# Kernel tuning notes

Hardware: AMD Instinct MI355X
Metric: run time of the kernel (lower is better)

## Reference

```python
import jax, jax.numpy as jnp
import numpy as np

N_NODES = 100000
N_EDGES = 1600000
N_FEAT = 48
N_EDGE_FEAT = 16
HIDDEN = 128


def setup_inputs() -> dict:
    key = jax.random.key(0)
    ks = jax.random.split(key, 8)
    tot = 2 * N_FEAT + N_EDGE_FEAT  # 112
    s1 = 1.0 / np.sqrt(tot)
    s2 = 1.0 / np.sqrt(HIDDEN)
    return {
        "x": jax.random.normal(ks[0], (N_NODES, N_FEAT), dtype=jnp.float32),
        "edge_index": jax.random.randint(ks[1], (2, N_EDGES), 0, N_NODES, dtype=jnp.int64),
        "edge_feat": jax.random.normal(ks[2], (N_EDGES, N_EDGE_FEAT), dtype=jnp.float32),
        "W1": jax.random.normal(ks[3], (tot, HIDDEN), dtype=jnp.float32) * s1,
        "b1": jnp.zeros((HIDDEN,), dtype=jnp.float32),
        "W2": jax.random.normal(ks[4], (HIDDEN, HIDDEN), dtype=jnp.float32) * s2,
        "b2": jnp.zeros((HIDDEN,), dtype=jnp.float32),
        "W3": jax.random.normal(ks[5], (HIDDEN, N_FEAT), dtype=jnp.float32) * s2,
        "b3": jnp.zeros((N_FEAT,), dtype=jnp.float32),
    }


def reference(x, edge_index, edge_feat, W1, b1, W2, b2, W3, b3):
    source = edge_index[0]
    target = edge_index[1]
    # gather + concat: (n_edges, 2*n_feat + n_edge_feat)
    edge = jnp.concatenate([x[source], x[target], edge_feat], axis=-1)
    # 3-layer MLP with ReLU
    h = jax.nn.relu(edge @ W1 + b1)
    h = jax.nn.relu(h @ W2 + b2)
    message = h @ W3 + b3  # (n_edges, n_feat)
    # scatter-mean over target indices
    n = x.shape[0]
    msum = jax.ops.segment_sum(message, target, num_segments=n)
    cnt = jax.ops.segment_sum(jnp.ones((target.shape[0],), dtype=x.dtype), target, num_segments=n)
    update = msum / jnp.maximum(cnt, 1.0)[:, None]  # empty segments -> 0
    return x + update
```

## Files before the change

### kernel.cpp

```cpp
#include <hip/hip_runtime.h>
#include <hip/hip_bf16.h>


#define NN 100000
#define NE 1600000
#define NF 48
#define TOT 112
#define HID 128
#define TILE 256
#define NTILE 6250

typedef __attribute__((ext_vector_type(8))) short short8;
typedef __attribute__((ext_vector_type(4))) float floatx4;

__device__ __forceinline__ unsigned short f2bf(float f) {
    union { float f; unsigned u; } v; v.f = f;
    unsigned u = v.u;
    return (unsigned short)((u + 0x7FFFu + ((u >> 16) & 1u)) >> 16);
}
__device__ __forceinline__ unsigned pk2(float a, float b) {
    __hip_bfloat162 h = __float22bfloat162_rn(make_float2(a, b));
    return *(unsigned*)&h;
}

__global__ void hist_prep_kernel(const int* __restrict__ ei, int* __restrict__ cnt,
                                 const float* __restrict__ W1, const float* __restrict__ W2,
                                 const float* __restrict__ W3,
                                 unsigned short* __restrict__ wt1,
                                 unsigned short* __restrict__ wt2,
                                 unsigned short* __restrict__ wt3) {
    if (blockIdx.x < NTILE) {
        int e = blockIdx.x * 256 + threadIdx.x;
        atomicAdd(cnt + ei[NE + e], 1);
        return;
    }
    int idx = (blockIdx.x - NTILE) * 256 + threadIdx.x;
    if (idx < 16384) {
        int n = idx >> 7, k = idx & 127;
        wt1[idx] = (k < TOT) ? f2bf(W1[k * HID + n]) : (unsigned short)0;
    } else if (idx < 32768) {
        int j = idx - 16384; int n = j >> 7, k = j & 127;
        wt2[j] = f2bf(W2[k * HID + n]);
    } else if (idx < 38912) {
        int j = idx - 32768; int n = j >> 7, k = j & 127;
        wt3[j] = f2bf(W3[k * NF + n]);
    }
}

__global__ void scan_kernel(const int* __restrict__ cnt, int* __restrict__ off,
                            int* __restrict__ counter) {
    __shared__ int sd[256];
    __shared__ int sbase;
    int tid = threadIdx.x;
    int n = blockIdx.x * 256 + tid;
    int v = (n < NN) ? cnt[n] : 0;
    sd[tid] = v;
    __syncthreads();
#pragma unroll
    for (int d = 1; d < 256; d <<= 1) {
        int t = (tid >= d) ? sd[tid - d] : 0;
        __syncthreads();
        sd[tid] += t;
        __syncthreads();
    }
    if (tid == 255) sbase = atomicAdd(counter, sd[255]);
    __syncthreads();
    if (n < NN) off[n] = sbase + sd[tid] - v;
}

__global__ void place_kernel(const int* __restrict__ ei, int* __restrict__ off,
                             unsigned long long* __restrict__ srt) {
    int e = blockIdx.x * 256 + threadIdx.x;
    int t = ei[NE + e];
    int p = atomicAdd(off + t, 1);
    srt[p] = (unsigned long long)e | ((unsigned long long)ei[e] << 21) |
             ((unsigned long long)t << 38);
}

__device__ __forceinline__ const short8* frag_ptr(const unsigned short* base, int row, int s,
                                                  int lane15, int quad) {
    return (const short8*)((const char*)base + row * 256 + (((s * 4 + quad) ^ lane15) << 4));
}

__launch_bounds__(512, 2)
__global__ void gemm_kernel(const float* __restrict__ x, const float* __restrict__ ef,
                            const unsigned long long* __restrict__ srt,
                            const unsigned short* __restrict__ wt1,
                            const unsigned short* __restrict__ wt2,
                            const unsigned short* __restrict__ wt3,
                            const float* __restrict__ b1, const float* __restrict__ b2,
                            float* __restrict__ out_acc) {
    __shared__ __align__(16) unsigned short lw1[128 * 128];
    __shared__ __align__(16) unsigned short lw2[128 * 128];
    __shared__ __align__(16) unsigned short lw3[48 * 128];
    __shared__ __align__(16) unsigned short ea[TILE * 128];
    __shared__ float lb1[128], lb2[128];
    __shared__ int ltgt[TILE];
    __shared__ int seg_start[TILE + 4];
    __shared__ int seg_tgt[TILE];
    __shared__ int nseg;

    const int tid = threadIdx.x;
    const uint4* s1 = (const uint4*)wt1;
    for (int i = tid; i < 2048; i += 512) {
        int n = i >> 4, g = i & 15;
        *(uint4*)((char*)lw1 + n * 256 + ((g ^ (n & 15)) << 4)) = s1[i];
    }
    const uint4* s2 = (const uint4*)wt2;
    for (int i = tid; i < 2048; i += 512) {
        int n = i >> 4, g = i & 15;
        *(uint4*)((char*)lw2 + n * 256 + ((g ^ (n & 15)) << 4)) = s2[i];
    }
    const uint4* s3 = (const uint4*)wt3;
    for (int i = tid; i < 768; i += 512) {
        int n = i >> 4, g = i & 15;
        *(uint4*)((char*)lw3 + n * 256 + ((g ^ (n & 15)) << 4)) = s3[i];
    }
    if (tid < 128) lb1[tid] = b1[tid];
    else if (tid < 256) lb2[tid - 128] = b2[tid - 128];
    __syncthreads();

    const int l15 = tid & 15;
    const int q = (tid & 63) >> 4;
    const int ln = tid & 63;
    const int wave = tid >> 6;
    const int sub = ln & 1;
    const int grow = wave * 32 + (ln >> 1);
    const int gl15 = grow & 15;

    for (int tile = blockIdx.x; tile < NTILE; tile += gridDim.x) {
        const int e0 = tile * TILE;
        {
            unsigned long long pk = srt[e0 + grow];
            int eid = (int)(pk & 0x1FFFFFull);
            int src = (int)((pk >> 21) & 0x1FFFFull);
            int tgt = (int)(pk >> 38);
            if (sub == 0) ltgt[grow] = tgt;
            float4 v[14];
#pragma unroll
            for (int j = 0; j < 14; ++j) {
                int p = 2 * j + sub;
                const float4* gp;
                if (p < 12)      gp = (const float4*)(x + 48 * (size_t)src) + p;
                else if (p < 24) gp = (const float4*)(x + 48 * (size_t)tgt) + (p - 12);
                else             gp = (const float4*)(ef + 16 * (size_t)eid) + (p - 24);
                v[j] = *gp;
            }
#pragma unroll
            for (int j = 0; j < 14; ++j) {
                uint2 h = make_uint2(pk2(v[j].x, v[j].y), pk2(v[j].z, v[j].w));
                *(uint2*)((char*)ea + grow * 256 + ((j ^ gl15) << 4) + (sub << 3)) = h;
            }
            *(uint4*)((char*)ea + grow * 256 + (((14 + sub) ^ gl15) << 4)) =
                make_uint4(0u, 0u, 0u, 0u);
        }
#pragma unroll
        for (int layer = 0; layer < 2; ++layer) {
            const unsigned short* lw = layer ? lw2 : lw1;
            const float* lb = layer ? lb2 : lb1;
            short8 bf[2][4];
#pragma unroll
            for (int gi = 0; gi < 2; ++gi)
#pragma unroll
                for (int s = 0; s < 4; ++s)
                    bf[gi][s] = *frag_ptr(ea, (wave * 2 + gi) * 16 + l15, s, l15, q);
#pragma unroll
            for (int mt = 0; mt < 8; ++mt) {
                floatx4 a0 = (floatx4){0.f, 0.f, 0.f, 0.f};
                floatx4 a1 = (floatx4){0.f, 0.f, 0.f, 0.f};
#pragma unroll
                for (int s = 0; s < 4; ++s) {
                    short8 a = *frag_ptr(lw, mt * 16 + l15, s, l15, q);
                    a0 = __builtin_amdgcn_mfma_f32_16x16x32_bf16(a, bf[0][s], a0, 0, 0, 0);
                    a1 = __builtin_amdgcn_mfma_f32_16x16x32_bf16(a, bf[1][s], a1, 0, 0, 0);
                }
                int f0 = mt * 16 + q * 4;
                const float4 bv = *(const float4*)(lb + f0);
                uint2 h0 = make_uint2(pk2(fmaxf(a0[0] + bv.x, 0.f), fmaxf(a0[1] + bv.y, 0.f)),
                                      pk2(fmaxf(a0[2] + bv.z, 0.f), fmaxf(a0[3] + bv.w, 0.f)));
                uint2 h1 = make_uint2(pk2(fmaxf(a1[0] + bv.x, 0.f), fmaxf(a1[1] + bv.y, 0.f)),
                                      pk2(fmaxf(a1[2] + bv.z, 0.f), fmaxf(a1[3] + bv.w, 0.f)));
                int gran = 2 * mt + (q >> 1), off8 = (q & 1) << 3;
                *(uint2*)((char*)ea + (wave * 32 + l15) * 256 + ((gran ^ l15) << 4) + off8) = h0;
                *(uint2*)((char*)ea + (wave * 32 + 16 + l15) * 256 + ((gran ^ l15) << 4) + off8) = h1;
            }
        }
        {
            short8 bf[2][4];
#pragma unroll
            for (int gi = 0; gi < 2; ++gi)
#pragma unroll
                for (int s = 0; s < 4; ++s)
                    bf[gi][s] = *frag_ptr(ea, (wave * 2 + gi) * 16 + l15, s, l15, q);
#pragma unroll
            for (int mt = 0; mt < 3; ++mt) {
                floatx4 a0 = (floatx4){0.f, 0.f, 0.f, 0.f};
                floatx4 a1 = (floatx4){0.f, 0.f, 0.f, 0.f};
#pragma unroll
                for (int s = 0; s < 4; ++s) {
                    short8 a = *frag_ptr(lw3, mt * 16 + l15, s, l15, q);
                    a0 = __builtin_amdgcn_mfma_f32_16x16x32_bf16(a, bf[0][s], a0, 0, 0, 0);
                    a1 = __builtin_amdgcn_mfma_f32_16x16x32_bf16(a, bf[1][s], a1, 0, 0, 0);
                }
                int gran = mt * 4 + q;
                *(float4*)((char*)ea + (wave * 32 + l15) * 256 + ((gran ^ l15) << 4)) =
                    *(float4*)&a0;
                *(float4*)((char*)ea + (wave * 32 + 16 + l15) * 256 + ((gran ^ l15) << 4)) =
                    *(float4*)&a1;
            }
        }
        __syncthreads();
        if (wave == 0) {
            int base = 0;
#pragma unroll
            for (int c = 0; c < 4; ++c) {
                int p = c * 64 + ln;
                int t = ltgt[p];
                int flag = (p == 0) || (t != ltgt[p - 1]);
                unsigned long long mask = __ballot(flag);
                int sid = base + __popcll(mask & ((1ull << ln) - 1ull));
                if (flag) { seg_start[sid] = p; seg_tgt[sid] = t; }
                base += __popcll(mask);
            }
            if (ln == 0) { nseg = base; seg_start[base] = TILE; }
        }
        __syncthreads();
        if (ln < 48) {
            const int gcol = ln >> 2, coff = (ln & 3) << 2;
            for (int s = wave; s < nseg; s += 8) {
                int a = seg_start[s], bnd = seg_start[s + 1];
                float s0 = 0.f, s1f = 0.f;
                int p = a;
                for (; p + 1 < bnd; p += 2) {
                    s0  += *(const float*)((const char*)ea + p * 256 +
                                           ((gcol ^ (p & 15)) << 4) + coff);
                    s1f += *(const float*)((const char*)ea + (p + 1) * 256 +
                                           ((gcol ^ ((p + 1) & 15)) << 4) + coff);
                }
                if (p < bnd)
                    s0 += *(const float*)((const char*)ea + p * 256 +
                                          ((gcol ^ (p & 15)) << 4) + coff);
                atomicAdd(out_acc + 48 * (size_t)seg_tgt[s] + ln, s0 + s1f);
            }
        }
        __syncthreads();
    }
}

__global__ void finalize_kernel(const float* __restrict__ x, const int* __restrict__ cnt,
                                const float* __restrict__ b3, float* __restrict__ out) {
    int i = blockIdx.x * 256 + threadIdx.x;
    float c = (float)cnt[i / 48];
    float upd = (c > 0.f) ? (out[i] / c + b3[i % 48]) : 0.f;
    out[i] = x[i] + upd;
}

extern "C" void kernel_launch(void* const* d_in, const int* in_sizes, int n_in,
                              void* d_out, int out_size, void* d_ws, size_t ws_size,
                              hipStream_t stream) {
    const float* x  = (const float*)d_in[0];
    const int*   ei = (const int*)d_in[1];
    const float* ef = (const float*)d_in[2];
    const float* W1 = (const float*)d_in[3];
    const float* b1 = (const float*)d_in[4];
    const float* W2 = (const float*)d_in[5];
    const float* b2 = (const float*)d_in[6];
    const float* W3 = (const float*)d_in[7];
    const float* b3 = (const float*)d_in[8];
    float* out = (float*)d_out;

    char* ws = (char*)d_ws;
    int* cnt     = (int*)ws;
    int* counter = (int*)(ws + 400000);
    int* off     = (int*)(ws + 409600);
    unsigned short* wt1 = (unsigned short*)(ws + 819456);
    unsigned short* wt2 = wt1 + 16384;
    unsigned short* wt3 = wt2 + 16384;
    unsigned long long* srt = (unsigned long long*)(ws + 901120);

    hipMemsetAsync(out, 0, (size_t)out_size * sizeof(float), stream);
    hipMemsetAsync(cnt, 0, (size_t)NN * sizeof(int) + 4, stream);
    hist_prep_kernel<<<NTILE + 152, 256, 0, stream>>>(ei, cnt, W1, W2, W3, wt1, wt2, wt3);
    scan_kernel<<<391, 256, 0, stream>>>(cnt, off, counter);
    place_kernel<<<6250, 256, 0, stream>>>(ei, off, srt);
    gemm_kernel<<<256, 512, 0, stream>>>(x, ef, srt, wt1, wt2, wt3, b1, b2, out);
    finalize_kernel<<<NN * NF / 256, 256, 0, stream>>>(x, cnt, b3, out);
}
```

Measured before the change: 592.9 us.

## Prefetch next tile's gather during MLP compute and drop interior-segment atomics

Software-pipelines the gemm kernel so the global gathers of x and edge features for the next tile are issued before the current tile's MFMA layers, hiding gather latency behind compute. It also raises wave priority during the MFMA section, replaces __syncthreads with a lighter LDS-wait barrier, and writes interior segment sums with plain stores, keeping atomics only for the first and last segment of each tile, which may straddle tile boundaries. The finalize kernel is vectorised to float4 and uses a reciprocal multiply. The prefetch keeps 14 float4 registers live across the MLP, which raises register pressure under the 512x2 launch bound. The plain-store path assumes no other tile writes interior targets, which holds because edges are sorted by target.

```diff
diff --git a/kernel.cpp b/kernel.cpp
--- a/kernel.cpp
+++ b/kernel.cpp
@@ -21,6 +21,11 @@
 __device__ __forceinline__ unsigned pk2(float a, float b) {
     __hip_bfloat162 h = __float22bfloat162_rn(make_float2(a, b));
     return *(unsigned*)&h;
+}
+
+__device__ __forceinline__ void bar_lgkm() {
+    asm volatile("s_waitcnt lgkmcnt(0)" ::: "memory");
+    __builtin_amdgcn_s_barrier();
 }
 
 __global__ void hist_prep_kernel(const int* __restrict__ ei, int* __restrict__ cnt,
@@ -80,6 +85,23 @@
 __device__ __forceinline__ const short8* frag_ptr(const unsigned short* base, int row, int s,
                                                   int lane15, int quad) {
     return (const short8*)((const char*)base + row * 256 + (((s * 4 + quad) ^ lane15) << 4));
+}
+
+__device__ __forceinline__ void gather_issue(const float* __restrict__ x,
+                                             const float* __restrict__ ef,
+                                             unsigned long long pk, int sub, float4* v) {
+    int eid = (int)(pk & 0x1FFFFFull);
+    int src = (int)((pk >> 21) & 0x1FFFFull);
+    int tgt = (int)(pk >> 38);
+#pragma unroll
+    for (int j = 0; j < 14; ++j) {
+        int p = 2 * j + sub;
+        const float4* gp;
+        if (p < 12)      gp = (const float4*)(x + 48 * (size_t)src) + p;
+        else if (p < 24) gp = (const float4*)(x + 48 * (size_t)tgt) + (p - 12);
+        else             gp = (const float4*)(ef + 16 * (size_t)eid) + (p - 24);
+        v[j] = *gp;
+    }
 }
 
 __launch_bounds__(512, 2)
@@ -127,25 +149,18 @@
     const int sub = ln & 1;
     const int grow = wave * 32 + (ln >> 1);
     const int gl15 = grow & 15;
-
-    for (int tile = blockIdx.x; tile < NTILE; tile += gridDim.x) {
-        const int e0 = tile * TILE;
+    const int G = gridDim.x;
+
+    unsigned long long pkCur = srt[(size_t)blockIdx.x * TILE + grow];
+    unsigned long long pkNext = (blockIdx.x + G < NTILE)
+        ? srt[(size_t)(blockIdx.x + G) * TILE + grow] : 0ull;
+    float4 v[14];
+    gather_issue(x, ef, pkCur, sub, v);
+
+    for (int tile = blockIdx.x; tile < NTILE; tile += G) {
         {
-            unsigned long long pk = srt[e0 + grow];
-            int eid = (int)(pk & 0x1FFFFFull);
-            int src = (int)((pk >> 21) & 0x1FFFFull);
-            int tgt = (int)(pk >> 38);
+            int tgt = (int)(pkCur >> 38);
             if (sub == 0) ltgt[grow] = tgt;
-            float4 v[14];
-#pragma unroll
-            for (int j = 0; j < 14; ++j) {
-                int p = 2 * j + sub;
-                const float4* gp;
-                if (p < 12)      gp = (const float4*)(x + 48 * (size_t)src) + p;
-                else if (p < 24) gp = (const float4*)(x + 48 * (size_t)tgt) + (p - 12);
-                else             gp = (const float4*)(ef + 16 * (size_t)eid) + (p - 24);
-                v[j] = *gp;
-            }
 #pragma unroll
             for (int j = 0; j < 14; ++j) {
                 uint2 h = make_uint2(pk2(v[j].x, v[j].y), pk2(v[j].z, v[j].w));
@@ -154,6 +169,18 @@
             *(uint4*)((char*)ea + grow * 256 + (((14 + sub) ^ gl15) << 4)) =
                 make_uint4(0u, 0u, 0u, 0u);
         }
+        {
+            unsigned long long pkN2 = 0ull;
+            if (tile + 2 * G < NTILE)
+                pkN2 = srt[(size_t)(tile + 2 * G) * TILE + grow];
+            if (tile + G < NTILE)
+                gather_issue(x, ef, pkNext, sub, v);
+            pkCur = pkNext;
+            pkNext = pkN2;
+        }
+        __builtin_amdgcn_sched_barrier(0);
+
+        __builtin_amdgcn_s_setprio(1);
 #pragma unroll
         for (int layer = 0; layer < 2; ++layer) {
             const unsigned short* lw = layer ? lw2 : lw1;
@@ -209,7 +236,8 @@
                     *(float4*)&a1;
             }
         }
-        __syncthreads();
+        __builtin_amdgcn_s_setprio(0);
+        bar_lgkm();
         if (wave == 0) {
             int base = 0;
 #pragma unroll
@@ -224,10 +252,11 @@
             }
             if (ln == 0) { nseg = base; seg_start[base] = TILE; }
         }
-        __syncthreads();
+        bar_lgkm();
         if (ln < 48) {
             const int gcol = ln >> 2, coff = (ln & 3) << 2;
-            for (int s = wave; s < nseg; s += 8) {
+            const int ns = nseg;
+            for (int s = wave; s < ns; s += 8) {
                 int a = seg_start[s], bnd = seg_start[s + 1];
                 float s0 = 0.f, s1f = 0.f;
                 int p = a;
@@ -240,19 +269,36 @@
                 if (p < bnd)
                     s0 += *(const float*)((const char*)ea + p * 256 +
                                           ((gcol ^ (p & 15)) << 4) + coff);
-                atomicAdd(out_acc + 48 * (size_t)seg_tgt[s] + ln, s0 + s1f);
-            }
-        }
-        __syncthreads();
+                float sum = s0 + s1f;
+                float* dst = out_acc + 48 * (size_t)seg_tgt[s] + ln;
+                if (s == 0 || s == ns - 1) atomicAdd(dst, sum);
+                else *dst = sum;
+            }
+        }
+        bar_lgkm();
     }
 }
 
 __global__ void finalize_kernel(const float* __restrict__ x, const int* __restrict__ cnt,
                                 const float* __restrict__ b3, float* __restrict__ out) {
     int i = blockIdx.x * 256 + threadIdx.x;
-    float c = (float)cnt[i / 48];
-    float upd = (c > 0.f) ? (out[i] / c + b3[i % 48]) : 0.f;
-    out[i] = x[i] + upd;
+    if (i >= NN * 12) return;
+    int node = i / 12, j = i % 12;
+    float c = (float)cnt[node];
+    float4 xv = ((const float4*)x)[i];
+    float4 ov = ((const float4*)out)[i];
+    float4 bv = ((const float4*)b3)[j];
+    float4 r;
+    if (c > 0.f) {
+        float rc = 1.f / c;
+        r.x = xv.x + ov.x * rc + bv.x;
+        r.y = xv.y + ov.y * rc + bv.y;
+        r.z = xv.z + ov.z * rc + bv.z;
+        r.w = xv.w + ov.w * rc + bv.w;
+    } else {
+        r = xv;
+    }
+    ((float4*)out)[i] = r;
 }
 
 extern "C" void kernel_launch(void* const* d_in, const int* in_sizes, int n_in,
@@ -284,5 +330,5 @@
     scan_kernel<<<391, 256, 0, stream>>>(cnt, off, counter);
     place_kernel<<<6250, 256, 0, stream>>>(ei, off, srt);
     gemm_kernel<<<256, 512, 0, stream>>>(x, ef, srt, wt1, wt2, wt3, b1, b2, out);
-    finalize_kernel<<<NN * NF / 256, 256, 0, stream>>>(x, cnt, b3, out);
-}
+    finalize_kernel<<<4688, 256, 0, stream>>>(x, cnt, b3, out);
+}
```

New measurement: 560.1 us. -5.5%, faster.
